# Optimization experiments

Hardware: AMD Instinct MI355X
Metric: run time of the kernel (lower is better)

The kernel has to match this reference:

```python
import jax, jax.numpy as jnp
import numpy as np

D_MODEL, D_STATE, D_CONV, EXPAND = 1024, 16, 4, 2
D_INNER = EXPAND * D_MODEL          # 2048
DT_RANK = D_MODEL // 16             # 64
B, L = 2, 1024


def setup_inputs() -> dict:
    key = jax.random.key(0)
    ks = jax.random.split(key, 10)
    x = jax.random.normal(ks[0], (B, L, D_MODEL), dtype=jnp.float32)
    ln_w = jnp.ones((D_MODEL,), jnp.float32)
    ln_b = jnp.zeros((D_MODEL,), jnp.float32)
    in_proj_w = jax.random.normal(ks[1], (2 * D_INNER, D_MODEL), jnp.float32) * (D_MODEL ** -0.5)
    conv_w = jax.random.normal(ks[2], (D_INNER, 1, D_CONV), jnp.float32) * (D_CONV ** -0.5)
    conv_b = jnp.zeros((D_INNER,), jnp.float32)
    x_proj_w = jax.random.normal(ks[3], (DT_RANK + 2 * D_STATE, D_INNER), jnp.float32) * (D_INNER ** -0.5)
    dt_proj_w = jax.random.normal(ks[4], (D_INNER, DT_RANK), jnp.float32) * (DT_RANK ** -0.5)
    # dt bias: inverse-softplus of dt sampled log-uniform in [1e-3, 1e-1] (mamba init)
    dt = jnp.exp(jax.random.uniform(ks[5], (D_INNER,)) * (np.log(0.1) - np.log(1e-3)) + np.log(1e-3))
    dt_proj_b = dt + jnp.log(-jnp.expm1(-dt))
    # A_log: log of [1..d_state] repeated per channel (S4D-real init)
    A_log = jnp.log(jnp.broadcast_to(jnp.arange(1, D_STATE + 1, dtype=jnp.float32), (D_INNER, D_STATE)))
    D = jnp.ones((D_INNER,), jnp.float32)
    out_proj_w = jax.random.normal(ks[6], (D_MODEL, D_INNER), jnp.float32) * (D_INNER ** -0.5)
    return dict(x=x, ln_w=ln_w, ln_b=ln_b, in_proj_w=in_proj_w, conv_w=conv_w,
                conv_b=conv_b, x_proj_w=x_proj_w, dt_proj_w=dt_proj_w,
                dt_proj_b=dt_proj_b, A_log=A_log, D=D, out_proj_w=out_proj_w)


def _layernorm(x, w, b, eps=1e-5):
    mu = jnp.mean(x, axis=-1, keepdims=True)
    var = jnp.mean(jnp.square(x - mu), axis=-1, keepdims=True)
    return (x - mu) * jax.lax.rsqrt(var + eps) * w + b


def _mamba(h, in_proj_w, conv_w, conv_b, x_proj_w, dt_proj_w, dt_proj_b, A_log, D, out_proj_w):
    # h: (B, L, d_model)
    xz = jnp.einsum('bld,ed->ble', h, in_proj_w)          # (B,L,2*d_inner)
    x_in, z = jnp.split(xz, 2, axis=-1)                   # each (B,L,d_inner)
    # depthwise causal conv1d
    kernel = jnp.transpose(conv_w, (2, 1, 0))             # (d_conv, 1, d_inner) LIO
    x_conv = jax.lax.conv_general_dilated(
        x_in, kernel, window_strides=(1,), padding=[(D_CONV - 1, 0)],
        dimension_numbers=('NLC', 'LIO', 'NLC'), feature_group_count=D_INNER)
    x_conv = jax.nn.silu(x_conv + conv_b)                 # (B,L,d_inner)
    # input-dependent SSM parameters
    x_dbl = jnp.einsum('bld,ed->ble', x_conv, x_proj_w)   # (B,L,dt_rank+2*d_state)
    dt, B_ssm, C_ssm = jnp.split(x_dbl, [DT_RANK, DT_RANK + D_STATE], axis=-1)
    dt = jax.nn.softplus(jnp.einsum('blr,dr->bld', dt, dt_proj_w) + dt_proj_b)  # (B,L,d_inner)
    A = -jnp.exp(A_log)                                   # (d_inner, d_state)
    deltaA = jnp.exp(dt[..., None] * A)                   # (B,L,d_inner,d_state)
    deltaBu = dt[..., None] * B_ssm[:, :, None, :] * x_conv[..., None]
    # selective scan: h_t = deltaA_t * h_{t-1} + deltaBu_t (parallel associative scan over L)
    def combine(left, right):
        a_l, b_l = left
        a_r, b_r = right
        return a_l * a_r, b_l * a_r + b_r
    _, states = jax.lax.associative_scan(combine, (deltaA, deltaBu), axis=1)
    y = jnp.einsum('blds,bls->bld', states, C_ssm) + x_conv * D
    y = y * jax.nn.silu(z)
    return jnp.einsum('bld,ed->ble', y, out_proj_w)       # (B,L,d_model)


def reference(x, ln_w, ln_b, in_proj_w, conv_w, conv_b, x_proj_w, dt_proj_w,
              dt_proj_b, A_log, D, out_proj_w):
    h = _layernorm(x, ln_w, ln_b)
    return x + _mamba(h, in_proj_w, conv_w, conv_b, x_proj_w, dt_proj_w,
                      dt_proj_b, A_log, D, out_proj_w)
```

## Files before the change

kernel.cpp:

```cpp
#include <hip/hip_runtime.h>
#include <hip/hip_bf16.h>
#include <math.h>

#define DM   1024
#define DI   2048
#define DS   16
#define DTR  64
#define NB   2
#define LL   1024
#define MR   (NB*LL)
#define XDBL 96
#define NC   32
#define CL   32

typedef _Float16 half8  __attribute__((ext_vector_type(8)));
typedef _Float16 half4v __attribute__((ext_vector_type(4)));
typedef float    floatx4 __attribute__((ext_vector_type(4)));

__device__ __forceinline__ void gload_lds16(const void* g, void* l) {
  __builtin_amdgcn_global_load_lds(
      (const __attribute__((address_space(1))) void*)g,
      (__attribute__((address_space(3))) void*)l, 16, 0, 0);
}

__global__ __launch_bounds__(256) void front_kernel(
    const float* __restrict__ x, const float* __restrict__ ln_w,
    const float* __restrict__ ln_b,
    const float* __restrict__ w_in, const float* __restrict__ w_out,
    const float* __restrict__ w_xp, const float* __restrict__ w_dt,
    _Float16* __restrict__ h_h,
    _Float16* __restrict__ w_in_h, _Float16* __restrict__ w_out_h,
    _Float16* __restrict__ w_xp_h, _Float16* __restrict__ w_dt_h,
    float* __restrict__ out, float* __restrict__ x_dbl) {
  const int blk = blockIdx.x;
  if (blk < MR) {
    __shared__ float sA[4], sB[4];
    const float* xr = x + (size_t)blk * DM;
    float s = 0.f, ss = 0.f;
    for (int i = threadIdx.x; i < DM; i += 256) {
      float v = xr[i];
      s += v; ss += v * v;
    }
    for (int o = 32; o > 0; o >>= 1) {
      s  += __shfl_down(s, o, 64);
      ss += __shfl_down(ss, o, 64);
    }
    const int wid = threadIdx.x >> 6, lid = threadIdx.x & 63;
    if (lid == 0) { sA[wid] = s; sB[wid] = ss; }
    __syncthreads();
    if (threadIdx.x == 0) {
      float S = sA[0] + sA[1] + sA[2] + sA[3];
      float SS = sB[0] + sB[1] + sB[2] + sB[3];
      float mu = S / DM;
      sA[0] = mu;
      sB[0] = rsqrtf(SS / DM - mu * mu + 1e-5f);
    }
    __syncthreads();
    const float mu = sA[0], rs = sB[0];
    for (int i = threadIdx.x; i < DM; i += 256)
      h_h[(size_t)blk * DM + i] = (_Float16)((xr[i] - mu) * rs * ln_w[i] + ln_b[i]);
    return;
  }
  int i = (blk - MR) * 256 + threadIdx.x;
  const int N0 = 1048576, N1 = 524288, N2 = 49152, N3 = 32768, N4 = 524288, N5 = 49152;
  if (i < N0 + N1 + N2 + N3) {
    const float* s; _Float16* d; int off;
    if (i < N0)            { s = w_in;  d = w_in_h;  off = i; }
    else if (i < N0+N1)    { s = w_out; d = w_out_h; off = i - N0; }
    else if (i < N0+N1+N2) { s = w_xp;  d = w_xp_h;  off = i - N0 - N1; }
    else                   { s = w_dt;  d = w_dt_h;  off = i - N0 - N1 - N2; }
    float4 v = ((const float4*)s)[off];
    half4v h = {(_Float16)v.x, (_Float16)v.y, (_Float16)v.z, (_Float16)v.w};
    ((half4v*)d)[off] = h;
  } else if (i < N0+N1+N2+N3+N4) {
    int off = i - (N0+N1+N2+N3);
    ((float4*)out)[off] = ((const float4*)x)[off];
  } else if (i < N0+N1+N2+N3+N4+N5) {
    int off = i - (N0+N1+N2+N3+N4);
    ((float4*)x_dbl)[off] = make_float4(0.f, 0.f, 0.f, 0.f);
  }
}

__global__ __launch_bounds__(256) void dtext_kernel(
    const float* __restrict__ xdbl, _Float16* __restrict__ dtr) {
  int idx = blockIdx.x * 256 + threadIdx.x;
  int m = idx >> 6, c = idx & 63;
  dtr[idx] = (_Float16)xdbl[(size_t)m * XDBL + c];
}

template <int EPI, int TN>
__global__ __launch_bounds__(256) void gemm_mfma(
    const _Float16* __restrict__ A,
    const _Float16* __restrict__ W,
    void* __restrict__ Cv, void* __restrict__ C2v,
    const float* __restrict__ extra, int ldc,
    int M, int N, int K, int kchunk) {
  constexpr int NT = TN / 32;
  constexpr int WSLOT = TN / 16;
  __shared__ alignas(16) _Float16 As[128 * 32];
  __shared__ alignas(16) _Float16 Ws[TN * 32];
  const int t = threadIdx.x;
  const int wave = t >> 6, lane = t & 63;
  const int m0 = blockIdx.y * 128, n0 = blockIdx.x * TN;
  const int k_beg = blockIdx.z * kchunk;
  const int k_end = min(K, k_beg + kchunk);
  const int wm = (wave >> 1) * 64, wn = (wave & 1) * (TN / 2);
  floatx4 acc[4][NT];
#pragma unroll
  for (int i = 0; i < 4; i++)
#pragma unroll
    for (int j = 0; j < NT; j++) acc[i][j] = {0.f, 0.f, 0.f, 0.f};

  const int fr = lane & 15;
  const int kc8 = lane >> 4;

  for (int k0 = k_beg; k0 < k_end; k0 += 32) {
#pragma unroll
    for (int sl = wave; sl < 8; sl += 4) {
      const int idx = sl * 64 + lane;
      const int row = idx >> 2, kc = idx & 3;
      gload_lds16(A + (size_t)(m0 + row) * K + k0 + kc * 8, &As[sl * 512]);
    }
#pragma unroll
    for (int sl = wave; sl < WSLOT; sl += 4) {
      const int idx = sl * 64 + lane;
      const int row = idx >> 2, kc = idx & 3;
      const int wrow = (n0 + row < N) ? row : 0;
      gload_lds16(W + (size_t)(n0 + wrow) * K + k0 + kc * 8, &Ws[sl * 512]);
    }
    __syncthreads();
    half8 af[4], wf[NT];
#pragma unroll
    for (int i = 0; i < 4; i++)
      af[i] = *(const half8*)&As[(wm + i * 16 + fr) * 32 + kc8 * 8];
#pragma unroll
    for (int j = 0; j < NT; j++)
      wf[j] = *(const half8*)&Ws[(wn + j * 16 + fr) * 32 + kc8 * 8];
#pragma unroll
    for (int i = 0; i < 4; i++)
#pragma unroll
      for (int j = 0; j < NT; j++)
        acc[i][j] = __builtin_amdgcn_mfma_f32_16x16x32_f16(af[i], wf[j], acc[i][j], 0, 0, 0);
    __syncthreads();
  }

  const int col = lane & 15, rowq = lane >> 4;
#pragma unroll
  for (int i = 0; i < 4; i++) {
#pragma unroll
    for (int j = 0; j < NT; j++) {
      const int n = n0 + wn + j * 16 + col;
      if (n < N) {
#pragma unroll
        for (int r = 0; r < 4; r++) {
          const int m = m0 + wm + i * 16 + rowq * 4 + r;
          float v = acc[i][j][r];
          if (EPI == 0) {
            if (n < DI) ((_Float16*)Cv )[(size_t)m * DI + n]      = (_Float16)v;
            else        ((_Float16*)C2v)[(size_t)m * DI + n - DI] = (_Float16)v;
          } else if (EPI == 1) {
            v += extra[n];
            v = (v > 20.f) ? v : log1pf(expf(v));
            ((float*)Cv)[(size_t)m * ldc + n] = v;
          } else if (EPI == 3) {
            atomicAdd(&((float*)Cv)[(size_t)m * ldc + n], v);
          }
        }
      }
    }
  }
}

__global__ __launch_bounds__(256) void conv_silu_kernel(
    const _Float16* __restrict__ xin, const float* __restrict__ cw,
    const float* __restrict__ cb, _Float16* __restrict__ xc) {
  const int idx = blockIdx.x * 256 + threadIdx.x;
  const int d  = idx & (DI - 1);
  const int ml = idx >> 11;
  const int l  = ml & (LL - 1);
  float acc = cb[d];
#pragma unroll
  for (int k = 0; k < 4; k++) {
    int lp = l - 3 + k;
    if (lp >= 0)
      acc += (float)xin[(size_t)(ml - (3 - k)) * DI + d] * cw[d * 4 + k];
  }
  xc[idx] = (_Float16)(acc / (1.f + __expf(-acc)));
}

__device__ __forceinline__ bool load_a(const float* __restrict__ A_log, int d,
                                       float* a) {
  const float4* Ap = (const float4*)(A_log + (size_t)d * DS);
  bool fast = true;
#pragma unroll
  for (int i = 0; i < 4; i++) {
    float4 v = Ap[i];
    a[4 * i + 0] = -__expf(v.x); a[4 * i + 1] = -__expf(v.y);
    a[4 * i + 2] = -__expf(v.z); a[4 * i + 3] = -__expf(v.w);
  }
#pragma unroll
  for (int s = 0; s < DS; s++)
    fast = fast && (fabsf(a[s] + (float)(s + 1)) < 1e-4f);
  return fast;
}

__global__ __launch_bounds__(256) void scan_phase1(
    const _Float16* __restrict__ xc,
    const float* __restrict__ xdbl,
    const float* __restrict__ dtm,
    const float* __restrict__ A_log,
    float* __restrict__ HE,
    float* __restrict__ SA) {
  __shared__ float Bs[CL][DS];
  const int bi = blockIdx.x;
  const int dblk = bi & 7;
  const int c = (bi >> 3) & (NC - 1);
  const int b = bi >> 8;
  const int t = threadIdx.x;
  const int d = dblk * 256 + t;
  const int mlbase = b * LL + c * CL;

  for (int i = t; i < CL * DS; i += 256) {
    int tt = i >> 4, s = i & 15;
    Bs[tt][s] = xdbl[(size_t)(mlbase + tt) * XDBL + DTR + s];
  }

  float a[DS];
  const bool fast = load_a(A_log, d, a);
  float h[DS];
#pragma unroll
  for (int s = 0; s < DS; s++) h[s] = 0.f;
  float S = 0.f;
  __syncthreads();

  if (fast) {
    for (int tt = 0; tt < CL; tt++) {
      const size_t ml = mlbase + tt;
      const float dtv = dtm[ml * DI + d];
      const float u   = (float)xc[ml * DI + d];
      const float du  = dtv * u;
      S += dtv;
      const float r = __expf(-dtv);
      float P = 1.f;
#pragma unroll
      for (int s = 0; s < DS; s++) {
        P *= r;
        h[s] = P * h[s] + du * Bs[tt][s];
      }
    }
  } else {
    for (int tt = 0; tt < CL; tt++) {
      const size_t ml = mlbase + tt;
      const float dtv = dtm[ml * DI + d];
      const float u   = (float)xc[ml * DI + d];
      const float du  = dtv * u;
      S += dtv;
#pragma unroll
      for (int s = 0; s < DS; s++)
        h[s] = __expf(dtv * a[s]) * h[s] + du * Bs[tt][s];
    }
  }
  const size_t base = ((size_t)(b * NC + c) * DS) * DI + d;
#pragma unroll
  for (int s = 0; s < DS; s++) HE[base + (size_t)s * DI] = h[s];
  SA[(size_t)(b * NC + c) * DI + d] = S;
}

__global__ __launch_bounds__(256) void scan_phase2(
    const float* __restrict__ A_log,
    const float* __restrict__ SA,
    float* __restrict__ HE) {
  const int idx = blockIdx.x * 256 + threadIdx.x;
  const int d = idx & (DI - 1);
  const int s = (idx >> 11) & (DS - 1);
  const int b = idx >> 15;
  const float a = -__expf(A_log[(size_t)d * DS + s]);
  float Hc = 0.f;
  for (int c = 0; c < NC; c++) {
    const size_t o = ((size_t)(b * NC + c) * DS + s) * DI + d;
    const float he = HE[o];
    const float P = __expf(a * SA[(size_t)(b * NC + c) * DI + d]);
    HE[o] = Hc;
    Hc = P * Hc + he;
  }
}

__global__ __launch_bounds__(256) void scan_phase3(
    const _Float16* __restrict__ xc,
    const float* __restrict__ xdbl,
    const float* __restrict__ dtm,
    const _Float16* __restrict__ zbuf,
    const float* __restrict__ A_log,
    const float* __restrict__ Dvec,
    const float* __restrict__ HE,
    _Float16* __restrict__ y) {
  __shared__ float Bs[CL][DS];
  __shared__ float Cs[CL][DS];
  const int bi = blockIdx.x;
  const int dblk = bi & 7;
  const int c = (bi >> 3) & (NC - 1);
  const int b = bi >> 8;
  const int t = threadIdx.x;
  const int d = dblk * 256 + t;
  const int mlbase = b * LL + c * CL;

  for (int i = t; i < CL * DS; i += 256) {
    int tt = i >> 4, s = i & 15;
    const size_t ro = (size_t)(mlbase + tt) * XDBL + DTR + s;
    Bs[tt][s] = xdbl[ro];
    Cs[tt][s] = xdbl[ro + DS];
  }

  float a[DS];
  const bool fast = load_a(A_log, d, a);
  float h[DS];
  const size_t base = ((size_t)(b * NC + c) * DS) * DI + d;
#pragma unroll
  for (int s = 0; s < DS; s++) h[s] = HE[base + (size_t)s * DI];
  const float Dv = Dvec[d];
  __syncthreads();

  if (fast) {
    for (int tt = 0; tt < CL; tt++) {
      const size_t ml = mlbase + tt;
      const float dtv = dtm[ml * DI + d];
      const float u   = (float)xc[ml * DI + d];
      const float du  = dtv * u;
      const float r = __expf(-dtv);
      float P = 1.f, p = 0.f;
#pragma unroll
      for (int s = 0; s < DS; s++) {
        P *= r;
        h[s] = P * h[s] + du * Bs[tt][s];
        p += h[s] * Cs[tt][s];
      }
      const float zv = (float)zbuf[ml * DI + d];
      const float sil = zv / (1.f + __expf(-zv));
      y[ml * DI + d] = (_Float16)((p + u * Dv) * sil);
    }
  } else {
    for (int tt = 0; tt < CL; tt++) {
      const size_t ml = mlbase + tt;
      const float dtv = dtm[ml * DI + d];
      const float u   = (float)xc[ml * DI + d];
      const float du  = dtv * u;
      float p = 0.f;
#pragma unroll
      for (int s = 0; s < DS; s++) {
        h[s] = __expf(dtv * a[s]) * h[s] + du * Bs[tt][s];
        p += h[s] * Cs[tt][s];
      }
      const float zv = (float)zbuf[ml * DI + d];
      const float sil = zv / (1.f + __expf(-zv));
      y[ml * DI + d] = (_Float16)((p + u * Dv) * sil);
    }
  }
}

extern "C" void kernel_launch(void* const* d_in, const int* in_sizes, int n_in,
                              void* d_out, int out_size, void* d_ws, size_t ws_size,
                              hipStream_t stream) {
  const float* x         = (const float*)d_in[0];
  const float* ln_w      = (const float*)d_in[1];
  const float* ln_b      = (const float*)d_in[2];
  const float* in_proj_w = (const float*)d_in[3];
  const float* conv_w    = (const float*)d_in[4];
  const float* conv_b    = (const float*)d_in[5];
  const float* x_proj_w  = (const float*)d_in[6];
  const float* dt_proj_w = (const float*)d_in[7];
  const float* dt_proj_b = (const float*)d_in[8];
  const float* A_log     = (const float*)d_in[9];
  const float* Dvec      = (const float*)d_in[10];
  const float* out_proj_w= (const float*)d_in[11];
  float* out = (float*)d_out;

  char* ws = (char*)d_ws;
  _Float16* h_h     = (_Float16*)ws;
  _Float16* xin_h   = (_Float16*)(ws + 4194304);
  _Float16* y_h     = xin_h;
  _Float16* z_h     = (_Float16*)(ws + 12582912);
  _Float16* xc_h    = (_Float16*)(ws + 20971520);
  float*    dtb     = (float*)   (ws + 29360128);
  float*    x_dbl   = (float*)   (ws + 46137344);
  float*    SA      = (float*)   (ws + 46923776);
  _Float16* dtr_h   = (_Float16*)(ws + 47448064);
  float*    HE      = (float*)   (ws + 47710208);
  _Float16* w_in_h  = (_Float16*)(ws + 56098816);
  _Float16* w_out_h = (_Float16*)(ws + 64487424);
  _Float16* w_xp_h  = (_Float16*)(ws + 68681728);
  _Float16* w_dt_h  = (_Float16*)(ws + 69074944);

  front_kernel<<<MR + 8704, 256, 0, stream>>>(
      x, ln_w, ln_b, in_proj_w, out_proj_w, x_proj_w, dt_proj_w,
      h_h, w_in_h, w_out_h, w_xp_h, w_dt_h, out, x_dbl);

  gemm_mfma<0, 64><<<dim3(2 * DI / 64, MR / 128, 1), 256, 0, stream>>>(
      h_h, w_in_h, xin_h, z_h, nullptr, 0, MR, 2 * DI, DM, DM);

  conv_silu_kernel<<<(MR * DI) / 256, 256, 0, stream>>>(xin_h, conv_w, conv_b, xc_h);

  gemm_mfma<3, 96><<<dim3(1, MR / 128, 16), 256, 0, stream>>>(
      xc_h, w_xp_h, x_dbl, nullptr, nullptr, XDBL, MR, XDBL, DI, DI / 16);

  dtext_kernel<<<(MR * DTR) / 256, 256, 0, stream>>>(x_dbl, dtr_h);
  gemm_mfma<1, 64><<<dim3(DI / 64, MR / 128, 1), 256, 0, stream>>>(
      dtr_h, w_dt_h, dtb, nullptr, dt_proj_b, DI, MR, DI, DTR, DTR);

  scan_phase1<<<NB * NC * (DI / 256), 256, 0, stream>>>(
      xc_h, x_dbl, dtb, A_log, HE, SA);
  scan_phase2<<<(NB * DS * DI) / 256, 256, 0, stream>>>(A_log, SA, HE);
  scan_phase3<<<NB * NC * (DI / 256), 256, 0, stream>>>(
      xc_h, x_dbl, dtb, z_h, A_log, Dvec, HE, y_h);

  gemm_mfma<3, 64><<<dim3(DM / 64, MR / 128, 4), 256, 0, stream>>>(
      y_h, w_out_h, out, nullptr, nullptr, DM, MR, DM, DI, DI / 4);
}
```

Before: 269.5 us.

## Double-buffer GEMM LDS tiles, replace split-K atomics with partial buffers, vectorize conv

The GEMM kernel now double-buffers its LDS tiles, issuing the next k-tile's global loads before computing the current one and dropping one barrier per iteration. Split-K atomicAdd epilogues are replaced by per-split partial buffers plus dedicated reduction kernels. The x_proj reduction also emits the dt slice in fp16, folding away dtext_kernel, and the out_proj reduction adds the residual, so front_kernel no longer copies x into out or zeroes x_dbl. The out_proj split-K drops from 4 to 2, and conv_silu processes 8 channels per thread with vector loads. These changes add two extra launches and extra partial-buffer traffic, and double the LDS use per block.

```diff
diff --git a/kernel.cpp b/kernel.cpp
--- a/kernel.cpp
+++ b/kernel.cpp
@@ -30,8 +30,7 @@
     const float* __restrict__ w_xp, const float* __restrict__ w_dt,
     _Float16* __restrict__ h_h,
     _Float16* __restrict__ w_in_h, _Float16* __restrict__ w_out_h,
-    _Float16* __restrict__ w_xp_h, _Float16* __restrict__ w_dt_h,
-    float* __restrict__ out, float* __restrict__ x_dbl) {
+    _Float16* __restrict__ w_xp_h, _Float16* __restrict__ w_dt_h) {
   const int blk = blockIdx.x;
   if (blk < MR) {
     __shared__ float sA[4], sB[4];
@@ -62,30 +61,16 @@
     return;
   }
   int i = (blk - MR) * 256 + threadIdx.x;
-  const int N0 = 1048576, N1 = 524288, N2 = 49152, N3 = 32768, N4 = 524288, N5 = 49152;
-  if (i < N0 + N1 + N2 + N3) {
-    const float* s; _Float16* d; int off;
-    if (i < N0)            { s = w_in;  d = w_in_h;  off = i; }
-    else if (i < N0+N1)    { s = w_out; d = w_out_h; off = i - N0; }
-    else if (i < N0+N1+N2) { s = w_xp;  d = w_xp_h;  off = i - N0 - N1; }
-    else                   { s = w_dt;  d = w_dt_h;  off = i - N0 - N1 - N2; }
-    float4 v = ((const float4*)s)[off];
-    half4v h = {(_Float16)v.x, (_Float16)v.y, (_Float16)v.z, (_Float16)v.w};
-    ((half4v*)d)[off] = h;
-  } else if (i < N0+N1+N2+N3+N4) {
-    int off = i - (N0+N1+N2+N3);
-    ((float4*)out)[off] = ((const float4*)x)[off];
-  } else if (i < N0+N1+N2+N3+N4+N5) {
-    int off = i - (N0+N1+N2+N3+N4);
-    ((float4*)x_dbl)[off] = make_float4(0.f, 0.f, 0.f, 0.f);
-  }
-}
-
-__global__ __launch_bounds__(256) void dtext_kernel(
-    const float* __restrict__ xdbl, _Float16* __restrict__ dtr) {
-  int idx = blockIdx.x * 256 + threadIdx.x;
-  int m = idx >> 6, c = idx & 63;
-  dtr[idx] = (_Float16)xdbl[(size_t)m * XDBL + c];
+  const int N0 = 1048576, N1 = 524288, N2 = 49152, N3 = 32768;
+  const float* s; _Float16* d; int off;
+  if (i < N0)            { s = w_in;  d = w_in_h;  off = i; }
+  else if (i < N0+N1)    { s = w_out; d = w_out_h; off = i - N0; }
+  else if (i < N0+N1+N2) { s = w_xp;  d = w_xp_h;  off = i - N0 - N1; }
+  else if (i < N0+N1+N2+N3) { s = w_dt; d = w_dt_h; off = i - N0 - N1 - N2; }
+  else return;
+  float4 v = ((const float4*)s)[off];
+  half4v h = {(_Float16)v.x, (_Float16)v.y, (_Float16)v.z, (_Float16)v.w};
+  ((half4v*)d)[off] = h;
 }
 
 template <int EPI, int TN>
@@ -97,13 +82,13 @@
     int M, int N, int K, int kchunk) {
   constexpr int NT = TN / 32;
   constexpr int WSLOT = TN / 16;
-  __shared__ alignas(16) _Float16 As[128 * 32];
-  __shared__ alignas(16) _Float16 Ws[TN * 32];
+  __shared__ alignas(16) _Float16 As[2][128 * 32];
+  __shared__ alignas(16) _Float16 Ws[2][TN * 32];
   const int t = threadIdx.x;
   const int wave = t >> 6, lane = t & 63;
   const int m0 = blockIdx.y * 128, n0 = blockIdx.x * TN;
   const int k_beg = blockIdx.z * kchunk;
-  const int k_end = min(K, k_beg + kchunk);
+  const int nk = kchunk >> 5;
   const int wm = (wave >> 1) * 64, wn = (wave & 1) * (TN / 2);
   floatx4 acc[4][NT];
 #pragma unroll
@@ -114,34 +99,38 @@
   const int fr = lane & 15;
   const int kc8 = lane >> 4;
 
-  for (int k0 = k_beg; k0 < k_end; k0 += 32) {
-#pragma unroll
+  auto stage = [&](int buf, int k0) {
     for (int sl = wave; sl < 8; sl += 4) {
       const int idx = sl * 64 + lane;
       const int row = idx >> 2, kc = idx & 3;
-      gload_lds16(A + (size_t)(m0 + row) * K + k0 + kc * 8, &As[sl * 512]);
-    }
-#pragma unroll
+      gload_lds16(A + (size_t)(m0 + row) * K + k0 + kc * 8, &As[buf][sl * 512]);
+    }
     for (int sl = wave; sl < WSLOT; sl += 4) {
       const int idx = sl * 64 + lane;
       const int row = idx >> 2, kc = idx & 3;
       const int wrow = (n0 + row < N) ? row : 0;
-      gload_lds16(W + (size_t)(n0 + wrow) * K + k0 + kc * 8, &Ws[sl * 512]);
-    }
+      gload_lds16(W + (size_t)(n0 + wrow) * K + k0 + kc * 8, &Ws[buf][sl * 512]);
+    }
+  };
+
+  stage(0, k_beg);
+  int cur = 0;
+  for (int ki = 0; ki < nk; ki++) {
     __syncthreads();
+    if (ki + 1 < nk) stage(cur ^ 1, k_beg + ((ki + 1) << 5));
     half8 af[4], wf[NT];
 #pragma unroll
     for (int i = 0; i < 4; i++)
-      af[i] = *(const half8*)&As[(wm + i * 16 + fr) * 32 + kc8 * 8];
+      af[i] = *(const half8*)&As[cur][(wm + i * 16 + fr) * 32 + kc8 * 8];
 #pragma unroll
     for (int j = 0; j < NT; j++)
-      wf[j] = *(const half8*)&Ws[(wn + j * 16 + fr) * 32 + kc8 * 8];
+      wf[j] = *(const half8*)&Ws[cur][(wn + j * 16 + fr) * 32 + kc8 * 8];
 #pragma unroll
     for (int i = 0; i < 4; i++)
 #pragma unroll
       for (int j = 0; j < NT; j++)
         acc[i][j] = __builtin_amdgcn_mfma_f32_16x16x32_f16(af[i], wf[j], acc[i][j], 0, 0, 0);
-    __syncthreads();
+    cur ^= 1;
   }
 
   const int col = lane & 15, rowq = lane >> 4;
@@ -162,30 +151,64 @@
             v += extra[n];
             v = (v > 20.f) ? v : log1pf(expf(v));
             ((float*)Cv)[(size_t)m * ldc + n] = v;
-          } else if (EPI == 3) {
-            atomicAdd(&((float*)Cv)[(size_t)m * ldc + n], v);
+          } else if (EPI == 4) {
+            ((float*)Cv)[((size_t)blockIdx.z * M + m) * ldc + n] = v;
           }
         }
       }
     }
   }
+}
+
+__global__ __launch_bounds__(256) void xproj_reduce(
+    const float* __restrict__ part,
+    float* __restrict__ x_dbl, _Float16* __restrict__ dtr) {
+  const int idx = blockIdx.x * 256 + threadIdx.x;
+  const int m = idx / XDBL, c = idx - m * XDBL;
+  float s = 0.f;
+#pragma unroll
+  for (int z = 0; z < 16; z++) s += part[(size_t)z * (MR * XDBL) + idx];
+  x_dbl[idx] = s;
+  if (c < DTR) dtr[m * DTR + c] = (_Float16)s;
+}
+
+__global__ __launch_bounds__(256) void out_reduce(
+    const float* __restrict__ x, const float* __restrict__ part,
+    float* __restrict__ out) {
+  const int i = blockIdx.x * 256 + threadIdx.x;
+  float4 a  = ((const float4*)x)[i];
+  float4 p0 = ((const float4*)part)[i];
+  float4 p1 = ((const float4*)(part + (size_t)MR * DM))[i];
+  float4 r = make_float4(a.x + p0.x + p1.x, a.y + p0.y + p1.y,
+                         a.z + p0.z + p1.z, a.w + p0.w + p1.w);
+  ((float4*)out)[i] = r;
 }
 
 __global__ __launch_bounds__(256) void conv_silu_kernel(
     const _Float16* __restrict__ xin, const float* __restrict__ cw,
     const float* __restrict__ cb, _Float16* __restrict__ xc) {
   const int idx = blockIdx.x * 256 + threadIdx.x;
-  const int d  = idx & (DI - 1);
-  const int ml = idx >> 11;
+  const int d8 = idx & (DI / 8 - 1);
+  const int ml = idx >> 8;
   const int l  = ml & (LL - 1);
-  float acc = cb[d];
+  const int d0 = d8 * 8;
+  half8 xr[4];
+  const half8 zero = {0, 0, 0, 0, 0, 0, 0, 0};
 #pragma unroll
   for (int k = 0; k < 4; k++) {
-    int lp = l - 3 + k;
-    if (lp >= 0)
-      acc += (float)xin[(size_t)(ml - (3 - k)) * DI + d] * cw[d * 4 + k];
-  }
-  xc[idx] = (_Float16)(acc / (1.f + __expf(-acc)));
+    const int lp = l - 3 + k;
+    xr[k] = (lp >= 0) ? *(const half8*)&xin[(size_t)(ml - 3 + k) * DI + d0] : zero;
+  }
+  half8 o;
+#pragma unroll
+  for (int j = 0; j < 8; j++) {
+    float acc = cb[d0 + j];
+#pragma unroll
+    for (int k = 0; k < 4; k++)
+      acc += (float)xr[k][j] * cw[(d0 + j) * 4 + k];
+    o[j] = (_Float16)(acc / (1.f + __expf(-acc)));
+  }
+  *(half8*)&xc[(size_t)ml * DI + d0] = o;
 }
 
 __device__ __forceinline__ bool load_a(const float* __restrict__ A_log, int d,
@@ -381,6 +404,7 @@
   _Float16* z_h     = (_Float16*)(ws + 12582912);
   _Float16* xc_h    = (_Float16*)(ws + 20971520);
   float*    dtb     = (float*)   (ws + 29360128);
+  float*    out_part= dtb;
   float*    x_dbl   = (float*)   (ws + 46137344);
   float*    SA      = (float*)   (ws + 46923776);
   _Float16* dtr_h   = (_Float16*)(ws + 47448064);
@@ -389,20 +413,21 @@
   _Float16* w_out_h = (_Float16*)(ws + 64487424);
   _Float16* w_xp_h  = (_Float16*)(ws + 68681728);
   _Float16* w_dt_h  = (_Float16*)(ws + 69074944);
-
-  front_kernel<<<MR + 8704, 256, 0, stream>>>(
+  float*    xp_part = (float*)   (ws + 69337088);
+
+  front_kernel<<<MR + 6464, 256, 0, stream>>>(
       x, ln_w, ln_b, in_proj_w, out_proj_w, x_proj_w, dt_proj_w,
-      h_h, w_in_h, w_out_h, w_xp_h, w_dt_h, out, x_dbl);
+      h_h, w_in_h, w_out_h, w_xp_h, w_dt_h);
 
   gemm_mfma<0, 64><<<dim3(2 * DI / 64, MR / 128, 1), 256, 0, stream>>>(
       h_h, w_in_h, xin_h, z_h, nullptr, 0, MR, 2 * DI, DM, DM);
 
-  conv_silu_kernel<<<(MR * DI) / 256, 256, 0, stream>>>(xin_h, conv_w, conv_b, xc_h);
-
-  gemm_mfma<3, 96><<<dim3(1, MR / 128, 16), 256, 0, stream>>>(
-      xc_h, w_xp_h, x_dbl, nullptr, nullptr, XDBL, MR, XDBL, DI, DI / 16);
-
-  dtext_kernel<<<(MR * DTR) / 256, 256, 0, stream>>>(x_dbl, dtr_h);
+  conv_silu_kernel<<<(MR * DI / 8) / 256, 256, 0, stream>>>(xin_h, conv_w, conv_b, xc_h);
+
+  gemm_mfma<4, 96><<<dim3(1, MR / 128, 16), 256, 0, stream>>>(
+      xc_h, w_xp_h, xp_part, nullptr, nullptr, XDBL, MR, XDBL, DI, DI / 16);
+  xproj_reduce<<<(MR * XDBL) / 256, 256, 0, stream>>>(xp_part, x_dbl, dtr_h);
+
   gemm_mfma<1, 64><<<dim3(DI / 64, MR / 128, 1), 256, 0, stream>>>(
       dtr_h, w_dt_h, dtb, nullptr, dt_proj_b, DI, MR, DI, DTR, DTR);
 
@@ -412,6 +437,7 @@
   scan_phase3<<<NB * NC * (DI / 256), 256, 0, stream>>>(
       xc_h, x_dbl, dtb, z_h, A_log, Dvec, HE, y_h);
 
-  gemm_mfma<3, 64><<<dim3(DM / 64, MR / 128, 4), 256, 0, stream>>>(
-      y_h, w_out_h, out, nullptr, nullptr, DM, MR, DM, DI, DI / 4);
-}
+  gemm_mfma<4, 64><<<dim3(DM / 64, MR / 128, 2), 256, 0, stream>>>(
+      y_h, w_out_h, out_part, nullptr, nullptr, DM, MR, DM, DI, DI / 2);
+  out_reduce<<<(MR * DM / 4) / 256, 256, 0, stream>>>(x, out_part, out);
+}
```

New measurement: 246.1 us. -8.7%, faster.
